# Kernel tuning notes

Hardware: AMD Instinct MI355X
Metric: run time of the kernel (lower is better)

Reference implementation:

```python
import jax, jax.numpy as jnp
import numpy as np

DIM = 96
D_STATE = 16
D_CONV = 3
D_INNER = 192   # int(DIM * 2.0)
DT_RANK = 6     # ceil(DIM / 16)
K = 4           # cross-scan directions
BATCH, H, W = 2, 56, 56


def setup_inputs() -> dict:
    key = jax.random.key(0)
    k = jax.random.split(key, 8)
    x = jax.random.normal(k[0], (BATCH, DIM, H, W), jnp.float32)
    W_in = jax.random.normal(k[1], (DIM, 2 * D_INNER), jnp.float32) / np.sqrt(DIM)
    W_conv = jax.random.normal(k[2], (D_INNER, 1, D_CONV, D_CONV), jnp.float32) / D_CONV
    b_conv = jnp.zeros((D_INNER,), jnp.float32)
    W_xproj = jax.random.normal(k[3], (K, D_INNER, DT_RANK + 2 * D_STATE), jnp.float32) / np.sqrt(D_INNER)
    W_dt = jax.random.normal(k[4], (K, DT_RANK, D_INNER), jnp.float32) / np.sqrt(DT_RANK)
    # dt bias init as in torch: dt ~ exp(U * (log 0.1 - log 0.001) + log 0.001), inv-softplus
    dt = jnp.exp(jax.random.uniform(k[5], (K, D_INNER), jnp.float32)
                 * (np.log(0.1) - np.log(0.001)) + np.log(0.001))
    dt = jnp.clip(dt, 1e-4, None)
    b_dt = dt + jnp.log(-jnp.expm1(-dt))
    A_logs = jnp.log(jnp.broadcast_to(jnp.arange(1, D_STATE + 1, dtype=jnp.float32),
                                      (K, D_INNER, D_STATE)))
    Ds = jnp.ones((K, D_INNER), jnp.float32)
    W_out = jax.random.normal(k[6], (D_INNER, DIM), jnp.float32) / np.sqrt(D_INNER)
    return dict(x=x, W_in=W_in, W_conv=W_conv, b_conv=b_conv, W_xproj=W_xproj,
                W_dt=W_dt, b_dt=b_dt, A_logs=A_logs, Ds=Ds, W_out=W_out)


def _ss2d(x, W_in, W_conv, b_conv, W_xproj, W_dt, b_dt, A_logs, Ds, W_out):
    Bsz, C, Hh, Ww = x.shape
    L = Hh * Ww
    # in_proj
    xf = x.transpose(0, 2, 3, 1).reshape(Bsz, L, C)        # (B, L, C)
    xz = xf @ W_in
    xp, z = jnp.split(xz, 2, axis=-1)                       # each (B, L, D)
    # depthwise conv + silu
    xi = xp.reshape(Bsz, Hh, Ww, -1).transpose(0, 3, 1, 2)  # (B, D, H, W)
    pad = D_CONV // 2
    xi = jax.lax.conv_general_dilated(
        xi, W_conv, (1, 1), ((pad, pad), (pad, pad)),
        feature_group_count=xi.shape[1],
        dimension_numbers=('NCHW', 'OIHW', 'NCHW')) + b_conv[None, :, None, None]
    xi = jax.nn.silu(xi)
    D = xi.shape[1]
    # cross-scan: 4 directions, each (B, L, D)
    x1 = xi.reshape(Bsz, D, L).transpose(0, 2, 1)
    x2 = xi[:, :, :, ::-1].reshape(Bsz, D, L).transpose(0, 2, 1)
    xt = xi.transpose(0, 1, 3, 2)                           # (B, D, W, H)
    x3 = xt.reshape(Bsz, D, L).transpose(0, 2, 1)
    x4 = xt[:, :, :, ::-1].reshape(Bsz, D, L).transpose(0, 2, 1)
    xs = jnp.stack([x1, x2, x3, x4])                        # (K, B, L, D)
    # per-direction projections, batched over K
    xdbl = jnp.einsum('kbld,kde->kble', xs, W_xproj)
    dr = xdbl[..., :DT_RANK]
    Bk = xdbl[..., DT_RANK:DT_RANK + D_STATE]               # (K, B, L, N)
    Ck = xdbl[..., DT_RANK + D_STATE:]                      # (K, B, L, N)
    delta = jax.nn.softplus(jnp.einsum('kblr,krd->kbld', dr, W_dt)
                            + b_dt[:, None, None, :])       # (K, B, L, D)
    A = -jnp.exp(A_logs)                                    # (K, D, N)

    def step(h, inp):
        x_i, d_i, B_i, C_i = inp  # (K,B,D), (K,B,D), (K,B,N), (K,B,N)
        dA = jnp.exp(d_i[..., None] * A[:, None])           # (K, B, D, N)
        h = dA * h + (d_i * x_i)[..., None] * B_i[:, :, None, :]
        y = jnp.einsum('kbdn,kbn->kbd', h, C_i)
        return h, y

    h0 = jnp.zeros((K, Bsz, D, D_STATE), xs.dtype)
    seq = (xs.transpose(2, 0, 1, 3), delta.transpose(2, 0, 1, 3),
           Bk.transpose(2, 0, 1, 3), Ck.transpose(2, 0, 1, 3))
    _, ys = jax.lax.scan(step, h0, seq)                     # (L, K, B, D)
    ys = ys.transpose(1, 2, 0, 3) + xs * Ds[:, None, None, :]  # (K, B, L, D)
    # cross-merge back to row-major (h w) order
    y1 = ys[0]
    y2 = ys[1].reshape(Bsz, Hh, Ww, D)[:, :, ::-1, :].reshape(Bsz, L, D)
    y3 = ys[2].reshape(Bsz, Ww, Hh, D).transpose(0, 2, 1, 3).reshape(Bsz, L, D)
    y4 = ys[3].reshape(Bsz, Ww, Hh, D)[:, :, ::-1, :].transpose(0, 2, 1, 3).reshape(Bsz, L, D)
    y = (y1 + y2 + y3 + y4) * jax.nn.silu(z)
    out = (y @ W_out).reshape(Bsz, Hh, Ww, C).transpose(0, 3, 1, 2)
    return out


def reference(x, W_in, W_conv, b_conv, W_xproj, W_dt, b_dt, A_logs, Ds, W_out):
    return _ss2d(x, W_in, W_conv, b_conv, W_xproj, W_dt, b_dt, A_logs, Ds, W_out)
```

## Files before the change

### kernel.cpp

```cpp
#include <hip/hip_runtime.h>
#include <math.h>

constexpr int BATCH  = 2;
constexpr int CDIM   = 96;
constexpr int HH     = 56;
constexpr int WW     = 56;
constexpr int LL     = HH * WW;
constexpr int DIN    = 192;
constexpr int NK     = 4;
constexpr int NST    = 16;
constexpr int RNK    = 6;
constexpr int EPROJ  = RNK + 2 * NST;
constexpr int SCH    = 64;
constexpr int NCH    = LL / SCH;
constexpr int CGRP   = DIN / 16;

constexpr int STDU = SCH + 2;
constexpr int STBC = SCH + 6;
constexpr int STY  = SCH + 4;
constexpr int STB1 = SCH + 4;

constexpr size_t SZ_PX   = (size_t)BATCH * LL * DIN;
constexpr size_t OFF_XP  = 0;
constexpr size_t OFF_Z   = OFF_XP + SZ_PX;
constexpr size_t OFF_XI  = OFF_Z  + SZ_PX;
constexpr size_t OFF_DR  = OFF_XI + SZ_PX;
constexpr size_t SZ_DR   = (size_t)NK * BATCH * LL * 8;
constexpr size_t OFF_B   = OFF_DR + SZ_DR;
constexpr size_t SZ_BC   = (size_t)NK * BATCH * LL * NST;
constexpr size_t OFF_C   = OFF_B + SZ_BC;
constexpr size_t OFF_YD  = OFF_C + SZ_BC;
constexpr size_t SZ_YD   = (size_t)NK * BATCH * LL * DIN;
constexpr size_t OFF_HE  = OFF_YD + SZ_YD;
constexpr size_t SZ_HS   = (size_t)NK * BATCH * NCH * DIN * NST;
constexpr size_t OFF_WT  = OFF_HE + 2 * SZ_HS;
constexpr size_t SZ_WT   = (size_t)NK * EPROJ * DIN;

__device__ __forceinline__ float silu(float v) {
    return v / (1.0f + __expf(-v));
}

__device__ __forceinline__ float softplus_f(float x) {
    return (x > 20.0f) ? x : __logf(1.0f + __expf(x));
}

__device__ __forceinline__ int seq_to_lr(int k, int l) {
    int q = l / WW;
    int r = l - q * WW;
    if (k == 0) return l;
    if (k == 1) return q * WW + (WW - 1 - r);
    if (k == 2) return r * WW + q;
    return (WW - 1 - r) * WW + q;
}

__device__ __forceinline__ int spatial_to_seq(int k, int s) {
    int h = s / WW;
    int w = s - h * WW;
    if (k == 0) return s;
    if (k == 1) return h * WW + (WW - 1 - w);
    if (k == 2) return w * WW + h;
    return w * WW + (WW - 1 - h);
}

__device__ __forceinline__ size_t hs_idx(int c, int kb, int d, int n) {
    return ((size_t)(c * (NK * BATCH) + kb) * DIN + d) * NST + n;
}

__device__ __forceinline__ float4 delta4(
        float4 r03, float2 r45, const float4* wr, float4 bb4) {
    float4 raw = bb4;
    raw.x = fmaf(r03.x, wr[0].x, raw.x); raw.y = fmaf(r03.x, wr[0].y, raw.y);
    raw.z = fmaf(r03.x, wr[0].z, raw.z); raw.w = fmaf(r03.x, wr[0].w, raw.w);
    raw.x = fmaf(r03.y, wr[1].x, raw.x); raw.y = fmaf(r03.y, wr[1].y, raw.y);
    raw.z = fmaf(r03.y, wr[1].z, raw.z); raw.w = fmaf(r03.y, wr[1].w, raw.w);
    raw.x = fmaf(r03.z, wr[2].x, raw.x); raw.y = fmaf(r03.z, wr[2].y, raw.y);
    raw.z = fmaf(r03.z, wr[2].z, raw.z); raw.w = fmaf(r03.z, wr[2].w, raw.w);
    raw.x = fmaf(r03.w, wr[3].x, raw.x); raw.y = fmaf(r03.w, wr[3].y, raw.y);
    raw.z = fmaf(r03.w, wr[3].z, raw.z); raw.w = fmaf(r03.w, wr[3].w, raw.w);
    raw.x = fmaf(r45.x, wr[4].x, raw.x); raw.y = fmaf(r45.x, wr[4].y, raw.y);
    raw.z = fmaf(r45.x, wr[4].z, raw.z); raw.w = fmaf(r45.x, wr[4].w, raw.w);
    raw.x = fmaf(r45.y, wr[5].x, raw.x); raw.y = fmaf(r45.y, wr[5].y, raw.y);
    raw.z = fmaf(r45.y, wr[5].z, raw.z); raw.w = fmaf(r45.y, wr[5].w, raw.w);
    raw.x = softplus_f(raw.x); raw.y = softplus_f(raw.y);
    raw.z = softplus_f(raw.z); raw.w = softplus_f(raw.w);
    return raw;
}

constexpr int K1_PIX = 8;
__global__ __launch_bounds__(384) void k_inproj(
        const float* __restrict__ x, const float* __restrict__ W_in,
        const float* __restrict__ W_xproj,
        float* __restrict__ xp, float* __restrict__ z, float* __restrict__ Wt) {
    __shared__ float sxT[CDIM][K1_PIX];
    int gp0 = blockIdx.x * K1_PIX;
    int t   = threadIdx.x;
    int b   = gp0 / LL;
    int l0  = gp0 - b * LL;
    int gid = blockIdx.x * 384 + t;
    if (gid < NK * DIN * EPROJ) {
        int k = gid / (DIN * EPROJ);
        int r = gid % (DIN * EPROJ);
        int d = r / EPROJ;
        int e = r % EPROJ;
        Wt[((size_t)k * EPROJ + e) * DIN + d] = W_xproj[gid];
    }
    for (int i = t; i < CDIM * K1_PIX; i += 384) {
        int c = i >> 3, p = i & 7;
        sxT[c][p] = x[((size_t)(b * CDIM + c)) * LL + l0 + p];
    }
    __syncthreads();
    int e = t;
    float acc[K1_PIX];
#pragma unroll
    for (int p = 0; p < K1_PIX; p++) acc[p] = 0.0f;
    const float4* sx4 = (const float4*)sxT;
#pragma unroll 4
    for (int c = 0; c < CDIM; c++) {
        float w  = W_in[c * (2 * DIN) + e];
        float4 va = sx4[2 * c];
        float4 vb = sx4[2 * c + 1];
        acc[0] = fmaf(va.x, w, acc[0]); acc[1] = fmaf(va.y, w, acc[1]);
        acc[2] = fmaf(va.z, w, acc[2]); acc[3] = fmaf(va.w, w, acc[3]);
        acc[4] = fmaf(vb.x, w, acc[4]); acc[5] = fmaf(vb.y, w, acc[5]);
        acc[6] = fmaf(vb.z, w, acc[6]); acc[7] = fmaf(vb.w, w, acc[7]);
    }
    if (e < DIN) {
#pragma unroll
        for (int p = 0; p < K1_PIX; p++)
            xp[((size_t)(gp0 + p)) * DIN + e] = acc[p];
    } else {
        int e2 = e - DIN;
#pragma unroll
        for (int p = 0; p < K1_PIX; p++)
            z[((size_t)(gp0 + p)) * DIN + e2] = acc[p];
    }
}

constexpr int KC_PIX = 4;
__global__ __launch_bounds__(192) void k_conv(
        const float* __restrict__ xp, const float* __restrict__ Wc,
        const float* __restrict__ bc, float* __restrict__ xi) {
    __shared__ float sW[9][DIN];
    int t = threadIdx.x;
    for (int i = t; i < DIN * 9; i += 192) {
        int d = i / 9, tap = i % 9;
        sW[tap][d] = Wc[i];
    }
    __syncthreads();
    int p   = t / 48;
    int cg4 = (t % 48) * 4;
    int gp  = blockIdx.x * KC_PIX + p;
    int b   = gp / LL;
    int l   = gp - b * LL;
    int h   = l / WW;
    int w   = l - h * WW;
    float4 acc = *(const float4*)&bc[cg4];
#pragma unroll
    for (int dy = -1; dy <= 1; dy++) {
        int hh = h + dy;
        if (hh < 0 || hh >= HH) continue;
#pragma unroll
        for (int dx = -1; dx <= 1; dx++) {
            int ww = w + dx;
            if (ww < 0 || ww >= WW) continue;
            float4 xv = *(const float4*)&xp[((size_t)b * LL + hh * WW + ww) * DIN + cg4];
            float4 wv = *(const float4*)&sW[(dy + 1) * 3 + (dx + 1)][cg4];
            acc.x = fmaf(xv.x, wv.x, acc.x);
            acc.y = fmaf(xv.y, wv.y, acc.y);
            acc.z = fmaf(xv.z, wv.z, acc.z);
            acc.w = fmaf(xv.w, wv.w, acc.w);
        }
    }
    float4 o;
    o.x = silu(acc.x); o.y = silu(acc.y); o.z = silu(acc.z); o.w = silu(acc.w);
    *(float4*)&xi[(size_t)gp * DIN + cg4] = o;
}

constexpr int K3_PIX = 32;
__global__ __launch_bounds__(256) void k_xproj(
        const float* __restrict__ xi, const float* __restrict__ Wt,
        float* __restrict__ drbuf, float* __restrict__ Bbuf,
        float* __restrict__ Cbuf) {
    __shared__ float4 v4[K3_PIX][49];
    int k   = blockIdx.y;
    int gp0 = blockIdx.x * K3_PIX;
    int b   = gp0 / LL;
    int l0  = gp0 - b * LL;
    int t   = threadIdx.x;
    const float4* xin4 = (const float4*)(xi + (size_t)gp0 * DIN);
    for (int i = t; i < K3_PIX * 48; i += 256)
        v4[i / 48][i % 48] = xin4[i];
    const float4* wt4 = (const float4*)(Wt + (size_t)k * EPROJ * DIN);
    __syncthreads();
    int p0 = t & 15;
    int eg = t >> 4;
    bool has3 = (eg < EPROJ - 32);
    float acc[2][3] = {{0.f, 0.f, 0.f}, {0.f, 0.f, 0.f}};
#pragma unroll 4
    for (int j = 0; j < 48; j++) {
        float4 w0 = wt4[eg * 48 + j];
        float4 w1 = wt4[(eg + 16) * 48 + j];
        float4 w2 = has3 ? wt4[(eg + 32) * 48 + j] : make_float4(0.f, 0.f, 0.f, 0.f);
#pragma unroll
        for (int q = 0; q < 2; q++) {
            float4 vv = v4[p0 + 16 * q][j];
            acc[q][0] = fmaf(vv.x, w0.x, acc[q][0]); acc[q][0] = fmaf(vv.y, w0.y, acc[q][0]);
            acc[q][0] = fmaf(vv.z, w0.z, acc[q][0]); acc[q][0] = fmaf(vv.w, w0.w, acc[q][0]);
            acc[q][1] = fmaf(vv.x, w1.x, acc[q][1]); acc[q][1] = fmaf(vv.y, w1.y, acc[q][1]);
            acc[q][1] = fmaf(vv.z, w1.z, acc[q][1]); acc[q][1] = fmaf(vv.w, w1.w, acc[q][1]);
            acc[q][2] = fmaf(vv.x, w2.x, acc[q][2]); acc[q][2] = fmaf(vv.y, w2.y, acc[q][2]);
            acc[q][2] = fmaf(vv.z, w2.z, acc[q][2]); acc[q][2] = fmaf(vv.w, w2.w, acc[q][2]);
        }
    }
#pragma unroll
    for (int q = 0; q < 2; q++) {
        int p  = p0 + 16 * q;
        int ls = spatial_to_seq(k, l0 + p);
        size_t kb  = (size_t)(k * BATCH + b);
        size_t b8  = (kb * LL + ls) * 8;
        size_t b16 = (kb * LL + ls) * NST;
        if (eg < RNK) drbuf[b8 + eg] = acc[q][0];
        else          Bbuf[b16 + eg - RNK] = acc[q][0];
        int e1 = eg + 16;
        if (e1 < RNK + NST) Bbuf[b16 + e1 - RNK] = acc[q][1];
        else                Cbuf[b16 + e1 - RNK - NST] = acc[q][1];
        if (has3) Cbuf[b16 + eg + 32 - RNK - NST] = acc[q][2];
    }
}

__global__ __launch_bounds__(256) void k_scanA(
        const float* __restrict__ xi, const float* __restrict__ drbuf,
        const float* __restrict__ Bbuf, const float* __restrict__ A_logs,
        const float* __restrict__ W_dt, const float* __restrict__ b_dt,
        float2* __restrict__ sum2) {
    __shared__ float2 sDU2[16][STDU];
    __shared__ float  sB1t[16][STB1];
    __shared__ float  sT[16][68];
    int c   = blockIdx.x;
    int blk = blockIdx.y;
    int k   = blk / (BATCH * CGRP);
    int rem = blk % (BATCH * CGRP);
    int b   = rem / CGRP;
    int cg  = rem % CGRP;
    int d0  = cg * 16;
    int t    = threadIdx.x;
    int lane = t & 63, wave = t >> 6;
    int grp  = lane >> 4, n = lane & 15;
    int ch   = wave * 4 + grp;
    int d    = d0 + ch;
    float A = -__expf(A_logs[((size_t)(k * DIN + d)) * NST + n]);
    size_t kb = (size_t)(k * BATCH + b);
    const float* drp = drbuf + kb * LL * 8;
    const float* bp  = Bbuf  + kb * LL * NST;
    const float* up  = xi    + (size_t)b * LL * DIN;
    int ss  = t >> 2;
    int cc0 = (t & 3) * 4;
    float4 wr[RNK];
#pragma unroll
    for (int r = 0; r < RNK; r++)
        wr[r] = *(const float4*)(W_dt + ((size_t)k * RNK + r) * DIN + d0 + cc0);
    float4 bb4 = *(const float4*)(b_dt + k * DIN + d0 + cc0);
    int l0 = c * SCH;
    {
        int l  = l0 + ss;
        int lr = seq_to_lr(k, l);
        float4 r03 = *(const float4*)(drp + (size_t)l * 8);
        float2 r45 = *(const float2*)(drp + (size_t)l * 8 + 4);
        float4 dlt = delta4(r03, r45, wr, bb4);
        float4 u4  = *(const float4*)(up + (size_t)lr * DIN + d0 + cc0);
        float4 B4  = *(const float4*)(bp + (size_t)l * NST + cc0);
        sDU2[cc0 + 0][ss] = make_float2(dlt.x, dlt.x * u4.x);
        sDU2[cc0 + 1][ss] = make_float2(dlt.y, dlt.y * u4.y);
        sDU2[cc0 + 2][ss] = make_float2(dlt.z, dlt.z * u4.z);
        sDU2[cc0 + 3][ss] = make_float2(dlt.w, dlt.w * u4.w);
        sB1t[cc0 + 0][ss] = B4.x;
        sB1t[cc0 + 1][ss] = B4.y;
        sB1t[cc0 + 2][ss] = B4.z;
        sB1t[cc0 + 3][ss] = B4.w;
    }
    __syncthreads();
    if (t < 16) {
        float run = 0.0f;
#pragma unroll 8
        for (int j = SCH - 1; j >= 0; j--) {
            sT[t][j] = run;
            run += sDU2[t][j].x;
        }
        sT[t][SCH] = run;
    }
    __syncthreads();
    float h0 = 0.f, h1 = 0.f, h2 = 0.f, h3 = 0.f;
#pragma unroll 2
    for (int j = 0; j < SCH; j += 4) {
        float4 tq  = *(const float4*)&sT[ch][j];
        float4 duA = *(const float4*)&sDU2[ch][j];
        float4 duB = *(const float4*)&sDU2[ch][j + 2];
        float4 bq  = *(const float4*)&sB1t[n][j];
        h0 = fmaf(__expf(A * tq.x), duA.y * bq.x, h0);
        h1 = fmaf(__expf(A * tq.y), duA.w * bq.y, h1);
        h2 = fmaf(__expf(A * tq.z), duB.y * bq.z, h2);
        h3 = fmaf(__expf(A * tq.w), duB.w * bq.w, h3);
    }
    float h = (h0 + h1) + (h2 + h3);
    float P = __expf(A * sT[ch][SCH]);
    sum2[hs_idx(c, (int)kb, d, n)] = make_float2(P, h);
}

__global__ __launch_bounds__(256) void k_scanC(
        const float* __restrict__ xi, const float* __restrict__ drbuf,
        const float* __restrict__ Bbuf, const float* __restrict__ Cbuf,
        const float* __restrict__ A_logs, const float* __restrict__ W_dt,
        const float* __restrict__ b_dt,
        const float2* __restrict__ sum2,
        float* __restrict__ ydir) {
    __shared__ float2 sDU2[16][STDU];
    __shared__ float2 sBC2[16][STBC];
    __shared__ float  sP[16 * 168];
    __shared__ float  sY[16][STY];
    int c   = blockIdx.x;
    int blk = blockIdx.y;
    int k   = blk / (BATCH * CGRP);
    int rem = blk % (BATCH * CGRP);
    int b   = rem / CGRP;
    int cg  = rem % CGRP;
    int d0  = cg * 16;
    int t    = threadIdx.x;
    int lane = t & 63, wave = t >> 6;
    int grp  = lane >> 4, n = lane & 15;
    int ch   = wave * 4 + grp;
    int d    = d0 + ch;
    float A = -__expf(A_logs[((size_t)(k * DIN + d)) * NST + n]);
    size_t kb = (size_t)(k * BATCH + b);
    const float* drp = drbuf + kb * LL * 8;
    const float* bp  = Bbuf  + kb * LL * NST;
    const float* cp  = Cbuf  + kb * LL * NST;
    const float* up  = xi    + (size_t)b * LL * DIN;
    float*       yp  = ydir  + kb * LL * DIN;
    float hin = 0.0f;
    {
        int j = 0;
        for (; j + 8 <= c; j += 8) {
            float2 a0 = sum2[hs_idx(j + 0, (int)kb, d, n)];
            float2 a1 = sum2[hs_idx(j + 1, (int)kb, d, n)];
            float2 a2 = sum2[hs_idx(j + 2, (int)kb, d, n)];
            float2 a3 = sum2[hs_idx(j + 3, (int)kb, d, n)];
            float2 a4 = sum2[hs_idx(j + 4, (int)kb, d, n)];
            float2 a5 = sum2[hs_idx(j + 5, (int)kb, d, n)];
            float2 a6 = sum2[hs_idx(j + 6, (int)kb, d, n)];
            float2 a7 = sum2[hs_idx(j + 7, (int)kb, d, n)];
            hin = fmaf(a0.x, hin, a0.y);
            hin = fmaf(a1.x, hin, a1.y);
            hin = fmaf(a2.x, hin, a2.y);
            hin = fmaf(a3.x, hin, a3.y);
            hin = fmaf(a4.x, hin, a4.y);
            hin = fmaf(a5.x, hin, a5.y);
            hin = fmaf(a6.x, hin, a6.y);
            hin = fmaf(a7.x, hin, a7.y);
        }
        for (; j < c; j++) {
            float2 a = sum2[hs_idx(j, (int)kb, d, n)];
            hin = fmaf(a.x, hin, a.y);
        }
    }
    int ss  = t >> 2;
    int cc0 = (t & 3) * 4;
    float4 wr[RNK];
#pragma unroll
    for (int r = 0; r < RNK; r++)
        wr[r] = *(const float4*)(W_dt + ((size_t)k * RNK + r) * DIN + d0 + cc0);
    float4 bb4 = *(const float4*)(b_dt + k * DIN + d0 + cc0);
    int l0 = c * SCH;
    {
        int l  = l0 + ss;
        int lr = seq_to_lr(k, l);
        float4 r03 = *(const float4*)(drp + (size_t)l * 8);
        float2 r45 = *(const float2*)(drp + (size_t)l * 8 + 4);
        float4 dlt = delta4(r03, r45, wr, bb4);
        float4 u4  = *(const float4*)(up + (size_t)lr * DIN + d0 + cc0);
        float4 B4  = *(const float4*)(bp + (size_t)l * NST + cc0);
        float4 C4  = *(const float4*)(cp + (size_t)l * NST + cc0);
        sDU2[cc0 + 0][ss] = make_float2(dlt.x, dlt.x * u4.x);
        sDU2[cc0 + 1][ss] = make_float2(dlt.y, dlt.y * u4.y);
        sDU2[cc0 + 2][ss] = make_float2(dlt.z, dlt.z * u4.z);
        sDU2[cc0 + 3][ss] = make_float2(dlt.w, dlt.w * u4.w);
        sBC2[cc0 + 0][ss] = make_float2(B4.x, C4.x);
        sBC2[cc0 + 1][ss] = make_float2(B4.y, C4.y);
        sBC2[cc0 + 2][ss] = make_float2(B4.z, C4.z);
        sBC2[cc0 + 3][ss] = make_float2(B4.w, C4.w);
    }
    __syncthreads();
    float h = hin;
    int pbase = ch * 168 + n;
    for (int w8 = 0; w8 < 8; w8++) {
        int sbase = w8 * 8;
#pragma unroll
        for (int si = 0; si < 8; si += 2) {
            float4 du = *(const float4*)&sDU2[ch][sbase + si];
            float4 bc = *(const float4*)&sBC2[n][sbase + si];
            float dA0 = __expf(du.x * A);
            h = fmaf(dA0, h, du.y * bc.x);
            sP[pbase + si * 20] = h * bc.y;
            float dA1 = __expf(du.z * A);
            h = fmaf(dA1, h, du.w * bc.z);
            sP[pbase + (si + 1) * 20] = h * bc.w;
        }
        __builtin_amdgcn_wave_barrier();
        if (lane < 32) {
            int chc = (wave << 2) + (lane >> 3);
            int sw  = lane & 7;
            const float4* pr = (const float4*)&sP[chc * 168 + sw * 20];
            float4 a = pr[0], b4 = pr[1], c4 = pr[2], e4 = pr[3];
            float4 s1, s2;
            s1.x = a.x + b4.x; s1.y = a.y + b4.y; s1.z = a.z + b4.z; s1.w = a.w + b4.w;
            s2.x = c4.x + e4.x; s2.y = c4.y + e4.y; s2.z = c4.z + e4.z; s2.w = c4.w + e4.w;
            s1.x += s2.x; s1.y += s2.y; s1.z += s2.z; s1.w += s2.w;
            sY[chc][sbase + sw] = (s1.x + s1.y) + (s1.z + s1.w);
        }
        __builtin_amdgcn_wave_barrier();
    }
    __syncthreads();
    {
        int s  = t >> 2;
        int c4 = (t & 3) * 4;
        int lr = seq_to_lr(k, l0 + s);
        float4 v = make_float4(sY[c4 + 0][s], sY[c4 + 1][s],
                               sY[c4 + 2][s], sY[c4 + 3][s]);
        *(float4*)&yp[(size_t)lr * DIN + d0 + c4] = v;
    }
}

constexpr int K5_PIX = 8;
__global__ __launch_bounds__(192) void k_out(
        const float* __restrict__ ydir, const float* __restrict__ xi,
        const float* __restrict__ zbuf, const float* __restrict__ Ds,
        const float* __restrict__ W_out, float* __restrict__ out) {
    __shared__ float g[DIN][12];
    __shared__ float so[CDIM][9];
    int gp0 = blockIdx.x * K5_PIX;
    int b   = gp0 / LL;
    int l0  = gp0 - b * LL;
    int t   = threadIdx.x;
    for (int i = t; i < K5_PIX * DIN; i += 192) {
        int p = i / DIN, dd = i % DIN;
        size_t off = (size_t)(gp0 + p) * DIN + dd;
        float y = ydir[off] + ydir[SZ_PX + off]
                + ydir[2 * SZ_PX + off] + ydir[3 * SZ_PX + off];
        float dsum = Ds[dd] + Ds[DIN + dd] + Ds[2 * DIN + dd] + Ds[3 * DIN + dd];
        y = fmaf(xi[off], dsum, y);
        g[dd][p] = y * silu(zbuf[off]);
    }
    __syncthreads();
    int f    = t % CDIM;
    int half = t / CDIM;
    float acc[4] = {0.f, 0.f, 0.f, 0.f};
#pragma unroll 4
    for (int dd = 0; dd < DIN; dd++) {
        float wv = W_out[dd * CDIM + f];
        float4 gv = *(const float4*)&g[dd][half * 4];
        acc[0] = fmaf(gv.x, wv, acc[0]);
        acc[1] = fmaf(gv.y, wv, acc[1]);
        acc[2] = fmaf(gv.z, wv, acc[2]);
        acc[3] = fmaf(gv.w, wv, acc[3]);
    }
#pragma unroll
    for (int p = 0; p < 4; p++) so[f][half * 4 + p] = acc[p];
    __syncthreads();
    for (int i = t; i < CDIM * K5_PIX; i += 192) {
        int f2 = i / K5_PIX, p2 = i % K5_PIX;
        out[((size_t)(b * CDIM + f2)) * LL + l0 + p2] = so[f2][p2];
    }
}

extern "C" void kernel_launch(void* const* d_in, const int* in_sizes, int n_in,
                              void* d_out, int out_size, void* d_ws, size_t ws_size,
                              hipStream_t stream) {
    const float* x       = (const float*)d_in[0];
    const float* W_in    = (const float*)d_in[1];
    const float* W_conv  = (const float*)d_in[2];
    const float* b_conv  = (const float*)d_in[3];
    const float* W_xproj = (const float*)d_in[4];
    const float* W_dt    = (const float*)d_in[5];
    const float* b_dt    = (const float*)d_in[6];
    const float* A_logs  = (const float*)d_in[7];
    const float* Ds      = (const float*)d_in[8];
    const float* W_out   = (const float*)d_in[9];
    float* out = (float*)d_out;
    float* ws  = (float*)d_ws;

    float* xp    = ws + OFF_XP;
    float* z     = ws + OFF_Z;
    float* xi    = ws + OFF_XI;
    float* drbuf = ws + OFF_DR;
    float* Bbuf  = ws + OFF_B;
    float* Cbuf  = ws + OFF_C;
    float* ydir  = ws + OFF_YD;
    float2* sum2 = (float2*)(ws + OFF_HE);
    float* Wt    = ws + OFF_WT;

    k_inproj<<<(BATCH * LL) / K1_PIX, 384, 0, stream>>>(x, W_in, W_xproj, xp, z, Wt);
    k_conv<<<(BATCH * LL) / KC_PIX, 192, 0, stream>>>(xp, W_conv, b_conv, xi);
    dim3 g3((BATCH * LL) / K3_PIX, NK);
    k_xproj<<<g3, 256, 0, stream>>>(xi, Wt, drbuf, Bbuf, Cbuf);
    dim3 gs(NCH, NK * BATCH * CGRP);
    k_scanA<<<gs, 256, 0, stream>>>(xi, drbuf, Bbuf, A_logs, W_dt, b_dt, sum2);
    k_scanC<<<gs, 256, 0, stream>>>(xi, drbuf, Bbuf, Cbuf, A_logs, W_dt, b_dt, sum2, ydir);
    k_out<<<(BATCH * LL) / K5_PIX, 192, 0, stream>>>(ydir, xi, z, Ds, W_out, out);
}
```

Baseline: 203.0 us.

## Restructure scan kernel: 4 states per thread, DPP reduction, 32 channels per block

The chunked scan pass now gives each thread four state entries of one channel instead of one state entry, so the 16-state C-dot reduction is done in registers plus two DPP cross-lane adds. This replaces the shared-memory partial-product buffer and its wave-level reduction. Blocks now cover 32 channels with 128 threads, and B/C are staged once per timestep as float4 rows. The change cuts shared traffic and reduction overhead, but it launches fewer threads in total and lengthens each thread's serial dependency chain.

```diff
diff --git a/kernel.cpp b/kernel.cpp
--- a/kernel.cpp
+++ b/kernel.cpp
@@ -14,10 +14,10 @@
 constexpr int SCH    = 64;
 constexpr int NCH    = LL / SCH;
 constexpr int CGRP   = DIN / 16;
+constexpr int C_DPB  = 32;
+constexpr int C_NBLK = DIN / C_DPB;
 
 constexpr int STDU = SCH + 2;
-constexpr int STBC = SCH + 6;
-constexpr int STY  = SCH + 4;
 constexpr int STB1 = SCH + 4;
 
 constexpr size_t SZ_PX   = (size_t)BATCH * LL * DIN;
@@ -306,126 +306,127 @@
     sum2[hs_idx(c, (int)kb, d, n)] = make_float2(P, h);
 }
 
-__global__ __launch_bounds__(256) void k_scanC(
+__global__ __launch_bounds__(128) void k_scanC(
         const float* __restrict__ xi, const float* __restrict__ drbuf,
         const float* __restrict__ Bbuf, const float* __restrict__ Cbuf,
         const float* __restrict__ A_logs, const float* __restrict__ W_dt,
         const float* __restrict__ b_dt,
         const float2* __restrict__ sum2,
         float* __restrict__ ydir) {
-    __shared__ float2 sDU2[16][STDU];
-    __shared__ float2 sBC2[16][STBC];
-    __shared__ float  sP[16 * 168];
-    __shared__ float  sY[16][STY];
+    __shared__ float2 sDU2[C_DPB][65];
+    __shared__ float4 sB4[SCH][5];
+    __shared__ float4 sC4[SCH][5];
+    __shared__ float  sY[C_DPB][65];
     int c   = blockIdx.x;
     int blk = blockIdx.y;
-    int k   = blk / (BATCH * CGRP);
-    int rem = blk % (BATCH * CGRP);
-    int b   = rem / CGRP;
-    int cg  = rem % CGRP;
-    int d0  = cg * 16;
+    int k   = blk / (BATCH * C_NBLK);
+    int rem = blk % (BATCH * C_NBLK);
+    int b   = rem / C_NBLK;
+    int g   = rem % C_NBLK;
+    int d0  = g * C_DPB;
     int t    = threadIdx.x;
     int lane = t & 63, wave = t >> 6;
-    int grp  = lane >> 4, n = lane & 15;
-    int ch   = wave * 4 + grp;
-    int d    = d0 + ch;
-    float A = -__expf(A_logs[((size_t)(k * DIN + d)) * NST + n]);
+    int dl   = wave * 16 + (lane >> 2);
+    int ng   = lane & 3;
+    int n0   = ng * 4;
+    int d    = d0 + dl;
     size_t kb = (size_t)(k * BATCH + b);
     const float* drp = drbuf + kb * LL * 8;
     const float* bp  = Bbuf  + kb * LL * NST;
     const float* cp  = Cbuf  + kb * LL * NST;
     const float* up  = xi    + (size_t)b * LL * DIN;
     float*       yp  = ydir  + kb * LL * DIN;
-    float hin = 0.0f;
+    float4 al = *(const float4*)(A_logs + ((size_t)(k * DIN + d)) * NST + n0);
+    float A0 = -__expf(al.x), A1 = -__expf(al.y);
+    float A2 = -__expf(al.z), A3 = -__expf(al.w);
+    float h0 = 0.f, h1 = 0.f, h2 = 0.f, h3 = 0.f;
     {
         int j = 0;
-        for (; j + 8 <= c; j += 8) {
-            float2 a0 = sum2[hs_idx(j + 0, (int)kb, d, n)];
-            float2 a1 = sum2[hs_idx(j + 1, (int)kb, d, n)];
-            float2 a2 = sum2[hs_idx(j + 2, (int)kb, d, n)];
-            float2 a3 = sum2[hs_idx(j + 3, (int)kb, d, n)];
-            float2 a4 = sum2[hs_idx(j + 4, (int)kb, d, n)];
-            float2 a5 = sum2[hs_idx(j + 5, (int)kb, d, n)];
-            float2 a6 = sum2[hs_idx(j + 6, (int)kb, d, n)];
-            float2 a7 = sum2[hs_idx(j + 7, (int)kb, d, n)];
-            hin = fmaf(a0.x, hin, a0.y);
-            hin = fmaf(a1.x, hin, a1.y);
-            hin = fmaf(a2.x, hin, a2.y);
-            hin = fmaf(a3.x, hin, a3.y);
-            hin = fmaf(a4.x, hin, a4.y);
-            hin = fmaf(a5.x, hin, a5.y);
-            hin = fmaf(a6.x, hin, a6.y);
-            hin = fmaf(a7.x, hin, a7.y);
+        for (; j + 4 <= c; j += 4) {
+            const float4* p0 = (const float4*)(sum2 + hs_idx(j + 0, (int)kb, d, n0));
+            const float4* p1 = (const float4*)(sum2 + hs_idx(j + 1, (int)kb, d, n0));
+            const float4* p2 = (const float4*)(sum2 + hs_idx(j + 2, (int)kb, d, n0));
+            const float4* p3 = (const float4*)(sum2 + hs_idx(j + 3, (int)kb, d, n0));
+            float4 a0 = p0[0], b0 = p0[1];
+            float4 a1 = p1[0], b1 = p1[1];
+            float4 a2 = p2[0], b2 = p2[1];
+            float4 a3 = p3[0], b3 = p3[1];
+            h0 = fmaf(a0.x, h0, a0.y); h1 = fmaf(a0.z, h1, a0.w);
+            h2 = fmaf(b0.x, h2, b0.y); h3 = fmaf(b0.z, h3, b0.w);
+            h0 = fmaf(a1.x, h0, a1.y); h1 = fmaf(a1.z, h1, a1.w);
+            h2 = fmaf(b1.x, h2, b1.y); h3 = fmaf(b1.z, h3, b1.w);
+            h0 = fmaf(a2.x, h0, a2.y); h1 = fmaf(a2.z, h1, a2.w);
+            h2 = fmaf(b2.x, h2, b2.y); h3 = fmaf(b2.z, h3, b2.w);
+            h0 = fmaf(a3.x, h0, a3.y); h1 = fmaf(a3.z, h1, a3.w);
+            h2 = fmaf(b3.x, h2, b3.y); h3 = fmaf(b3.z, h3, b3.w);
         }
         for (; j < c; j++) {
-            float2 a = sum2[hs_idx(j, (int)kb, d, n)];
-            hin = fmaf(a.x, hin, a.y);
-        }
-    }
-    int ss  = t >> 2;
-    int cc0 = (t & 3) * 4;
-    float4 wr[RNK];
-#pragma unroll
-    for (int r = 0; r < RNK; r++)
-        wr[r] = *(const float4*)(W_dt + ((size_t)k * RNK + r) * DIN + d0 + cc0);
-    float4 bb4 = *(const float4*)(b_dt + k * DIN + d0 + cc0);
+            const float4* pj = (const float4*)(sum2 + hs_idx(j, (int)kb, d, n0));
+            float4 a = pj[0], bq = pj[1];
+            h0 = fmaf(a.x, h0, a.y); h1 = fmaf(a.z, h1, a.w);
+            h2 = fmaf(bq.x, h2, bq.y); h3 = fmaf(bq.z, h3, bq.w);
+        }
+    }
     int l0 = c * SCH;
     {
+        int ss = t & 63;
+        int dg = t >> 6;
         int l  = l0 + ss;
         int lr = seq_to_lr(k, l);
         float4 r03 = *(const float4*)(drp + (size_t)l * 8);
         float2 r45 = *(const float2*)(drp + (size_t)l * 8 + 4);
-        float4 dlt = delta4(r03, r45, wr, bb4);
-        float4 u4  = *(const float4*)(up + (size_t)lr * DIN + d0 + cc0);
-        float4 B4  = *(const float4*)(bp + (size_t)l * NST + cc0);
-        float4 C4  = *(const float4*)(cp + (size_t)l * NST + cc0);
-        sDU2[cc0 + 0][ss] = make_float2(dlt.x, dlt.x * u4.x);
-        sDU2[cc0 + 1][ss] = make_float2(dlt.y, dlt.y * u4.y);
-        sDU2[cc0 + 2][ss] = make_float2(dlt.z, dlt.z * u4.z);
-        sDU2[cc0 + 3][ss] = make_float2(dlt.w, dlt.w * u4.w);
-        sBC2[cc0 + 0][ss] = make_float2(B4.x, C4.x);
-        sBC2[cc0 + 1][ss] = make_float2(B4.y, C4.y);
-        sBC2[cc0 + 2][ss] = make_float2(B4.z, C4.z);
-        sBC2[cc0 + 3][ss] = make_float2(B4.w, C4.w);
-    }
-    __syncthreads();
-    float h = hin;
-    int pbase = ch * 168 + n;
-    for (int w8 = 0; w8 < 8; w8++) {
-        int sbase = w8 * 8;
-#pragma unroll
-        for (int si = 0; si < 8; si += 2) {
-            float4 du = *(const float4*)&sDU2[ch][sbase + si];
-            float4 bc = *(const float4*)&sBC2[n][sbase + si];
-            float dA0 = __expf(du.x * A);
-            h = fmaf(dA0, h, du.y * bc.x);
-            sP[pbase + si * 20] = h * bc.y;
-            float dA1 = __expf(du.z * A);
-            h = fmaf(dA1, h, du.w * bc.z);
-            sP[pbase + (si + 1) * 20] = h * bc.w;
-        }
-        __builtin_amdgcn_wave_barrier();
-        if (lane < 32) {
-            int chc = (wave << 2) + (lane >> 3);
-            int sw  = lane & 7;
-            const float4* pr = (const float4*)&sP[chc * 168 + sw * 20];
-            float4 a = pr[0], b4 = pr[1], c4 = pr[2], e4 = pr[3];
-            float4 s1, s2;
-            s1.x = a.x + b4.x; s1.y = a.y + b4.y; s1.z = a.z + b4.z; s1.w = a.w + b4.w;
-            s2.x = c4.x + e4.x; s2.y = c4.y + e4.y; s2.z = c4.z + e4.z; s2.w = c4.w + e4.w;
-            s1.x += s2.x; s1.y += s2.y; s1.z += s2.z; s1.w += s2.w;
-            sY[chc][sbase + sw] = (s1.x + s1.y) + (s1.z + s1.w);
-        }
-        __builtin_amdgcn_wave_barrier();
-    }
-    __syncthreads();
-    {
-        int s  = t >> 2;
-        int c4 = (t & 3) * 4;
+#pragma unroll
+        for (int q = 0; q < 4; q++) {
+            int cc0 = dg * 16 + q * 4;
+            float4 wr[RNK];
+#pragma unroll
+            for (int r = 0; r < RNK; r++)
+                wr[r] = *(const float4*)(W_dt + ((size_t)k * RNK + r) * DIN + d0 + cc0);
+            float4 bb4 = *(const float4*)(b_dt + k * DIN + d0 + cc0);
+            float4 dlt = delta4(r03, r45, wr, bb4);
+            float4 u4  = *(const float4*)(up + (size_t)lr * DIN + d0 + cc0);
+            sDU2[cc0 + 0][ss] = make_float2(dlt.x, dlt.x * u4.x);
+            sDU2[cc0 + 1][ss] = make_float2(dlt.y, dlt.y * u4.y);
+            sDU2[cc0 + 2][ss] = make_float2(dlt.z, dlt.z * u4.z);
+            sDU2[cc0 + 3][ss] = make_float2(dlt.w, dlt.w * u4.w);
+        }
+        int s2 = t & 63;
+        int l2 = l0 + s2;
+        if (t < 64) {
+#pragma unroll
+            for (int q = 0; q < 4; q++)
+                sB4[s2][q] = *(const float4*)(bp + (size_t)l2 * NST + q * 4);
+        } else {
+#pragma unroll
+            for (int q = 0; q < 4; q++)
+                sC4[s2][q] = *(const float4*)(cp + (size_t)l2 * NST + q * 4);
+        }
+    }
+    __syncthreads();
+#pragma unroll 4
+    for (int s = 0; s < SCH; s++) {
+        float2 du = sDU2[dl][s];
+        float4 B4 = sB4[s][ng];
+        float4 C4 = sC4[s][ng];
+        h0 = fmaf(__expf(du.x * A0), h0, du.y * B4.x);
+        h1 = fmaf(__expf(du.x * A1), h1, du.y * B4.y);
+        h2 = fmaf(__expf(du.x * A2), h2, du.y * B4.z);
+        h3 = fmaf(__expf(du.x * A3), h3, du.y * B4.w);
+        float yq = (h0 * C4.x + h1 * C4.y) + (h2 * C4.z + h3 * C4.w);
+        yq += __int_as_float(__builtin_amdgcn_update_dpp(
+                0, __float_as_int(yq), 0xB1, 0xf, 0xf, true));
+        yq += __int_as_float(__builtin_amdgcn_update_dpp(
+                0, __float_as_int(yq), 0x4E, 0xf, 0xf, true));
+        if (ng == 0) sY[dl][s] = yq;
+    }
+    __syncthreads();
+    for (int i = t; i < SCH * (C_DPB / 4); i += 128) {
+        int dq = i & (C_DPB / 4 - 1);
+        int s  = i >> 3;
         int lr = seq_to_lr(k, l0 + s);
-        float4 v = make_float4(sY[c4 + 0][s], sY[c4 + 1][s],
-                               sY[c4 + 2][s], sY[c4 + 3][s]);
-        *(float4*)&yp[(size_t)lr * DIN + d0 + c4] = v;
+        float4 v = make_float4(sY[dq * 4 + 0][s], sY[dq * 4 + 1][s],
+                               sY[dq * 4 + 2][s], sY[dq * 4 + 3][s]);
+        *(float4*)&yp[(size_t)lr * DIN + d0 + dq * 4] = v;
     }
 }
 
@@ -501,8 +502,9 @@
     k_conv<<<(BATCH * LL) / KC_PIX, 192, 0, stream>>>(xp, W_conv, b_conv, xi);
     dim3 g3((BATCH * LL) / K3_PIX, NK);
     k_xproj<<<g3, 256, 0, stream>>>(xi, Wt, drbuf, Bbuf, Cbuf);
-    dim3 gs(NCH, NK * BATCH * CGRP);
-    k_scanA<<<gs, 256, 0, stream>>>(xi, drbuf, Bbuf, A_logs, W_dt, b_dt, sum2);
-    k_scanC<<<gs, 256, 0, stream>>>(xi, drbuf, Bbuf, Cbuf, A_logs, W_dt, b_dt, sum2, ydir);
+    dim3 gsA(NCH, NK * BATCH * CGRP);
+    k_scanA<<<gsA, 256, 0, stream>>>(xi, drbuf, Bbuf, A_logs, W_dt, b_dt, sum2);
+    dim3 gsC(NCH, NK * BATCH * C_NBLK);
+    k_scanC<<<gsC, 128, 0, stream>>>(xi, drbuf, Bbuf, Cbuf, A_logs, W_dt, b_dt, sum2, ydir);
     k_out<<<(BATCH * LL) / K5_PIX, 192, 0, stream>>>(ydir, xi, z, Ds, W_out, out);
 }
```

Result: no change. 206.0 us (+1.5%).
